# Kernel optimization log

Hardware: AMD Instinct MI355X
Metric: run time of the kernel (lower is better)

Reference implementation:

```python
import jax, jax.numpy as jnp
import numpy as np

B, S, D = 8, 1024, 128
EPS = 1e-7
LN_EPS = 1e-3  # keras LayerNormalization default


def setup_inputs() -> dict:
    key = jax.random.key(0)
    ks = jax.random.split(key, 8)
    sd = 1.0 / np.sqrt(D)
    return {
        "x": jax.random.normal(ks[0], (B, S, D), jnp.float32),
        "Wq": jax.random.normal(ks[1], (D, D), jnp.float32) * sd,
        "bq": jnp.zeros((D,), jnp.float32),
        "Wm": jax.random.normal(ks[2], (D, D), jnp.float32) * sd,
        "bm": jnp.zeros((D,), jnp.float32),
        "Ww": jax.random.normal(ks[3], (D, 1), jnp.float32) * sd,
        "bw": jnp.zeros((1,), jnp.float32),
        "Wc": jax.random.normal(ks[4], (D, 1), jnp.float32) * sd,
        "bc": jnp.zeros((1,), jnp.float32),
        "emb_map": jax.random.normal(ks[5], (D, D, D), jnp.float32) * 0.02,
        "gamma": jnp.ones((D,), jnp.float32),
        "beta": jnp.zeros((D,), jnp.float32),
    }


def reference(x, Wq, bq, Wm, bm, Ww, bw, Wc, bc, emb_map, gamma, beta):
    b_, s_, d_ = x.shape
    q = x @ Wq + bq                      # [B,S,D]
    m = jax.nn.sigmoid(x @ Wm + bm)      # [B,S,D]
    w = jax.nn.relu(x @ Ww + bw)         # [B,S,1]
    c = jax.nn.relu(x @ Wc + bc)         # [B,S,1]

    # distances: for query pos i, preceding pos j (j<i) has distance i-j
    idx = jnp.arange(s_)
    dist = (idx[:, None] - idx[None, :]).astype(x.dtype)   # [S,S]
    valid = dist > 0                                       # strict causal
    # cosh positional decay, zero outside causal window -> [B,S,S]
    pe = jnp.where(valid[None], 1.0 / jnp.cosh((dist[None] - c) / (w + EPS)), 0.0)

    # angle between (pe * x_j * m_i + eps) and (q_i + eps), expanded analytically
    qp = q + EPS
    t1 = jnp.einsum('bjd,bid->bij', x, m * qp)             # sum_d x_j m_i q'_i
    s1 = jnp.einsum('bjd,bid->bij', x, m)                  # sum_d x_j m_i
    s2 = jnp.einsum('bjd,bid->bij', x * x, m * m)          # sum_d (x_j m_i)^2
    dot = pe * t1 + EPS * jnp.sum(qp, axis=-1)[:, :, None]
    na = jnp.sqrt(pe * pe * s2 + 2.0 * EPS * pe * s1 + d_ * EPS * EPS)
    nb = jnp.linalg.norm(qp, axis=-1)[:, :, None]
    cos = jnp.where(valid[None], dot / (na * nb), 0.0)
    angle = jnp.where(valid[None], jnp.arccos(cos), 0.0)   # [B,S,S]

    # query_result_i = sum_j pe*angle * x_j  -> [B,S,D]
    qr = jnp.einsum('bij,bjd->bid', pe * angle, x)

    # embedding matrix: current_token (rows) outer query_result (cols),
    # contracted against rank-3 map: out[b,s,d] = sum_{j,k} x[b,s,j] qr[b,s,k] map[d,j,k]
    em = jnp.einsum('bsj,bsk->bsjk', x, qr).reshape(b_, s_, d_ * d_)
    mapped = em @ emb_map.reshape(d_, d_ * d_).T           # [B,S,D]

    res = mapped + x
    mu = jnp.mean(res, axis=-1, keepdims=True)
    var = jnp.var(res, axis=-1, keepdims=True)
    out = (res - mu) / jnp.sqrt(var + LN_EPS) * gamma + beta
    return out  # dropout is identity at inference
```

## Files before the change

### kernel.cpp

```cpp
#include <hip/hip_runtime.h>
#include <hip/hip_bf16.h>
#include <math.h>

#define DD 128
#define SS 1024
#define NROWS 8192
#define EPSF 1e-7f
#define LN_EPSF 1e-3f
#define TCUT 30.0f

typedef __attribute__((ext_vector_type(8))) short bf16x8;
typedef __attribute__((ext_vector_type(4))) float f32x4;
typedef __attribute__((ext_vector_type(16))) float f32x16;

__device__ __forceinline__ void gload_lds16(const void* g, void* l) {
    __builtin_amdgcn_global_load_lds(
        (const __attribute__((address_space(1))) unsigned int*)g,
        (__attribute__((address_space(3))) unsigned int*)l, 16, 0, 0);
}
__device__ __forceinline__ short f2bf(float v) {
    union { __hip_bfloat16 h; short s; } u;
    u.h = __float2bfloat16(v);
    return u.s;
}
__device__ __forceinline__ float bf2f(short s) {
    union { __hip_bfloat16 h; short s; } u; u.s = s;
    return __bfloat162float(u.h);
}
__device__ __forceinline__ unsigned int pack_bf16(float lo, float hi) {
    unsigned int r;
    asm("v_cvt_pk_bf16_f32 %0, %1, %2" : "=v"(r) : "v"(lo), "v"(hi));
    return r;
}
__device__ __forceinline__ float u2f(unsigned int u) {
    union { unsigned int u; float f; } c; c.u = u; return c.f;
}

__global__ __launch_bounds__(256) void k0a_emb(const float* __restrict__ emb,
                                               short* __restrict__ embh3) {
    __shared__ float lt[32][128];
    int d = blockIdx.x, js = blockIdx.y, t = threadIdx.x;
    {
        int jl = t >> 3, k0 = (t & 7) * 16;
        const float4* src = (const float4*)(emb + (size_t)d * 16384
                                            + (size_t)(js * 32 + jl) * 128 + k0);
#pragma unroll
        for (int q = 0; q < 4; ++q) *(float4*)&lt[jl][k0 + q * 4] = src[q];
    }
    __syncthreads();
    int ks = t >> 5, l0 = (t & 31) * 2;
    union { bf16x8 v[2]; short s[16]; } ob;
#pragma unroll
    for (int li = 0; li < 2; ++li) {
        int l = l0 + li;
        const float* p = &lt[l & 31][ks * 16 + (l >> 5) * 8];
#pragma unroll
        for (int e = 0; e < 8; ++e) ob.s[li * 8 + e] = f2bf(p[e]);
    }
    short* dst = embh3 + (size_t)(d * 4 + js) * 4096 + (size_t)t * 16;
    *(bf16x8*)dst = ob.v[0];
    *(bf16x8*)(dst + 8) = ob.v[1];
}

__global__ __launch_bounds__(256) void k0w_split(const float* __restrict__ Wq,
        const float* __restrict__ Wm, short* __restrict__ Wfrag) {
    int T = blockIdx.x * 256 + threadIdx.x;
    int e = T & 7, l = (T >> 3) & 63, ks = (T >> 9) & 3, nt = (T >> 11) & 7,
        mat = (T >> 14) & 1;
    int k = ks * 32 + ((l >> 4) & 3) * 8 + e;
    int c = nt * 16 + (l & 15);
    float v = (mat ? Wm : Wq)[k * 128 + c];
    short h = f2bf(v);
    float lo = v - bf2f(h);
    Wfrag[((((size_t)(mat * 2 + 0) * 8 + nt) * 4 + ks) * 64 + l) * 8 + e] = h;
    Wfrag[((((size_t)(mat * 2 + 1) * 8 + nt) * 4 + ks) * 64 + l) * 8 + e] = f2bf(lo);
}

__global__ __launch_bounds__(256) void k0c_xsplit(const float* __restrict__ x,
        const float* __restrict__ Ww, const float* __restrict__ bw,
        const float* __restrict__ Wc, const float* __restrict__ bc,
        short* __restrict__ xh2, short* __restrict__ xl2,
        float* __restrict__ scal) {
    __shared__ float xs[32][129];
    int rb = blockIdx.x, t = threadIdx.x;
    {
        int r = t >> 3, d0 = (t & 7) * 16;
        const float4* src = (const float4*)(x + (size_t)(rb * 32 + r) * 128 + d0);
#pragma unroll
        for (int q = 0; q < 4; ++q) *(float4*)&xs[r][d0 + q * 4] = src[q];
    }
    __syncthreads();
    int ks = (t >> 5) & 3, rf = t >> 7, l0 = (t & 31) * 2;
    union { bf16x8 v[2]; short s[16]; } hb, lb;
#pragma unroll
    for (int li = 0; li < 2; ++li) {
        int l = l0 + li;
        const float* p = &xs[rf * 16 + (l & 15)][ks * 32 + ((l >> 4) & 3) * 8];
#pragma unroll
        for (int e = 0; e < 8; ++e) {
            float v = p[e];
            short h = f2bf(v);
            hb.s[li * 8 + e] = h;
            lb.s[li * 8 + e] = f2bf(v - bf2f(h));
        }
    }
    {
        short* d1 = xh2 + (size_t)rb * 4096 + (size_t)t * 16;
        short* d2 = xl2 + (size_t)rb * 4096 + (size_t)t * 16;
        *(bf16x8*)d1 = hb.v[0]; *(bf16x8*)(d1 + 8) = hb.v[1];
        *(bf16x8*)d2 = lb.v[0]; *(bf16x8*)(d2 + 8) = lb.v[1];
    }
    int rr = t >> 3, seg = t & 7;
    float pw = 0.f, pc = 0.f;
#pragma unroll
    for (int dq = 0; dq < 16; ++dq) {
        float xv = xs[rr][seg * 16 + dq];
        pw = fmaf(xv, Ww[seg * 16 + dq], pw);
        pc = fmaf(xv, Wc[seg * 16 + dq], pc);
    }
    pw += __shfl_xor(pw, 1); pw += __shfl_xor(pw, 2); pw += __shfl_xor(pw, 4);
    pc += __shfl_xor(pc, 1); pc += __shfl_xor(pc, 2); pc += __shfl_xor(pc, 4);
    if (seg == 0) {
        scal[(size_t)(rb * 32 + rr) * 4 + 0] = fmaxf(pw + bw[0], 0.f);
        scal[(size_t)(rb * 32 + rr) * 4 + 1] = fmaxf(pc + bc[0], 0.f);
    }
}

__global__ __launch_bounds__(256) void k1_mfma(
    const short* __restrict__ xh2, const short* __restrict__ xl2,
    const short* __restrict__ Wfrag,
    const float* __restrict__ bq, const float* __restrict__ bm,
    float* __restrict__ mq, float* __restrict__ mo, float* __restrict__ scal)
{
    __shared__ __align__(16) short wl[65536];
    __shared__ float red[32][4][2];
    int t = threadIdx.x, w = t >> 6, l = t & 63;
    int l15 = l & 15, g = l >> 4;
    int row0 = blockIdx.x * 32;
#pragma unroll
    for (int it = 0; it < 32; ++it)
        gload_lds16(Wfrag + (size_t)(it * 256 + t) * 8, wl + (size_t)(it * 256 + w * 64) * 8);
    const short* xb  = xh2 + (size_t)blockIdx.x * 4096;
    const short* xlb = xl2 + (size_t)blockIdx.x * 4096;
    bf16x8 Ah[2][4], Al[2][4];
#pragma unroll
    for (int rf = 0; rf < 2; ++rf)
#pragma unroll
        for (int ks = 0; ks < 4; ++ks) {
            size_t o = ((size_t)(rf * 4 + ks) * 64 + l) * 8;
            Ah[rf][ks] = *(const bf16x8*)(xb + o);
            Al[rf][ks] = *(const bf16x8*)(xlb + o);
        }
    __syncthreads();
    f32x4 accq[2][2] = {}, accm[2][2] = {};
#pragma unroll
    for (int ntp = 0; ntp < 2; ++ntp) {
        int nt = w * 2 + ntp;
#pragma unroll
        for (int ks = 0; ks < 4; ++ks) {
            bf16x8 bhq = *(const bf16x8*)(wl + ((size_t)(0  + nt) * 4 + ks) * 512 + l * 8);
            bf16x8 blq = *(const bf16x8*)(wl + ((size_t)(8  + nt) * 4 + ks) * 512 + l * 8);
            bf16x8 bhm = *(const bf16x8*)(wl + ((size_t)(16 + nt) * 4 + ks) * 512 + l * 8);
            bf16x8 blm = *(const bf16x8*)(wl + ((size_t)(24 + nt) * 4 + ks) * 512 + l * 8);
#pragma unroll
            for (int rf = 0; rf < 2; ++rf) {
                accq[rf][ntp] = __builtin_amdgcn_mfma_f32_16x16x32_bf16(Ah[rf][ks], bhq, accq[rf][ntp], 0, 0, 0);
                accq[rf][ntp] = __builtin_amdgcn_mfma_f32_16x16x32_bf16(Ah[rf][ks], blq, accq[rf][ntp], 0, 0, 0);
                accq[rf][ntp] = __builtin_amdgcn_mfma_f32_16x16x32_bf16(Al[rf][ks], bhq, accq[rf][ntp], 0, 0, 0);
                accm[rf][ntp] = __builtin_amdgcn_mfma_f32_16x16x32_bf16(Ah[rf][ks], bhm, accm[rf][ntp], 0, 0, 0);
                accm[rf][ntp] = __builtin_amdgcn_mfma_f32_16x16x32_bf16(Ah[rf][ks], blm, accm[rf][ntp], 0, 0, 0);
                accm[rf][ntp] = __builtin_amdgcn_mfma_f32_16x16x32_bf16(Al[rf][ks], bhm, accm[rf][ntp], 0, 0, 0);
            }
        }
    }
    float sq1[2][4] = {{0,0,0,0},{0,0,0,0}};
    float sq2[2][4] = {{0,0,0,0},{0,0,0,0}};
#pragma unroll
    for (int ntp = 0; ntp < 2; ++ntp) {
        int c = (w * 2 + ntp) * 16 + l15;
        float bqv = bq[c] + EPSF, bmv = bm[c];
#pragma unroll
        for (int rf = 0; rf < 2; ++rf)
#pragma unroll
            for (int reg = 0; reg < 4; ++reg) {
                int rloc = rf * 16 + g * 4 + reg;
                float qp = accq[rf][ntp][reg] + bqv;
                float mv = 1.0f / (1.0f + expf(-(accm[rf][ntp][reg] + bmv)));
                size_t o = (size_t)(row0 + rloc) * 128 + c;
                mq[o] = mv * qp;
                mo[o] = mv;
                sq1[rf][reg] += qp;
                sq2[rf][reg] += qp * qp;
            }
    }
#pragma unroll
    for (int rf = 0; rf < 2; ++rf)
#pragma unroll
        for (int reg = 0; reg < 4; ++reg) {
            float a = sq1[rf][reg], b = sq2[rf][reg];
            a += __shfl_xor(a, 1); a += __shfl_xor(a, 2);
            a += __shfl_xor(a, 4); a += __shfl_xor(a, 8);
            b += __shfl_xor(b, 1); b += __shfl_xor(b, 2);
            b += __shfl_xor(b, 4); b += __shfl_xor(b, 8);
            if (l15 == 0) {
                red[rf * 16 + g * 4 + reg][w][0] = a;
                red[rf * 16 + g * 4 + reg][w][1] = b;
            }
        }
    __syncthreads();
    if (t < 32) {
        float a = red[t][0][0] + red[t][1][0] + red[t][2][0] + red[t][3][0];
        float b = red[t][0][1] + red[t][1][1] + red[t][2][1] + red[t][3][1];
        scal[(size_t)(row0 + t) * 4 + 2] = a;
        scal[(size_t)(row0 + t) * 4 + 3] = sqrtf(b);
    }
}

__global__ __launch_bounds__(256) void k2_qr(
    const float* __restrict__ x,
    const float* __restrict__ mq, const float* __restrict__ mo,
    const float* __restrict__ scal, short* __restrict__ qrh2)
{
    int row = blockIdx.x;
    int i = row & (SS - 1);
    const float* xb = x + (size_t)(row - i) * DD;
    int t = threadIdx.x, w = t >> 6, l = t & 63;
    int sub = l >> 4, q = l & 15;
    int qo = q * 8;

    float mqv[8], mov[8];
    {
        const float* mp = mq + (size_t)row * DD + qo;
        float4 a = *(const float4*)mp, b = *(const float4*)(mp + 4);
        mqv[0] = a.x; mqv[1] = a.y; mqv[2] = a.z; mqv[3] = a.w;
        mqv[4] = b.x; mqv[5] = b.y; mqv[6] = b.z; mqv[7] = b.w;
        const float* op = mo + (size_t)row * DD + qo;
        float4 c = *(const float4*)op, d = *(const float4*)(op + 4);
        mov[0] = c.x; mov[1] = c.y; mov[2] = c.z; mov[3] = c.w;
        mov[4] = d.x; mov[5] = d.y; mov[6] = d.z; mov[7] = d.w;
    }
    float wv = scal[row * 4 + 0], cv = scal[row * 4 + 1];
    float sumqp = scal[row * 4 + 2], nb = scal[row * 4 + 3];
    float wi = wv + EPSF;
    float dmaxf = cv + TCUT * wi;
    int dmax = (dmaxf >= (float)i) ? i : (int)dmaxf;

    float acc[8] = {0.f, 0.f, 0.f, 0.f, 0.f, 0.f, 0.f, 0.f};
    int nit = (dmax + 15) >> 4;
    int dbase = 1 + w * 4 + sub;
    for (int it = 0; it < nit; ++it) {
        int dist = dbase + it * 16;
        float xv[8];
        if (dist <= dmax) {
            const float* xp = xb + (size_t)(i - dist) * DD + qo;
            float4 a = *(const float4*)xp, b = *(const float4*)(xp + 4);
            xv[0] = a.x; xv[1] = a.y; xv[2] = a.z; xv[3] = a.w;
            xv[4] = b.x; xv[5] = b.y; xv[6] = b.z; xv[7] = b.w;
        } else {
#pragma unroll
            for (int e = 0; e < 8; ++e) xv[e] = 0.f;
        }
        float t1 = 0.f, s1 = 0.f, s2 = 0.f;
#pragma unroll
        for (int e = 0; e < 8; ++e) {
            float xm = xv[e] * mov[e];
            t1 = fmaf(xv[e], mqv[e], t1);
            s1 += xm;
            s2 = fmaf(xm, xm, s2);
        }
#pragma unroll
        for (int off = 1; off < 16; off <<= 1) {
            t1 += __shfl_xor(t1, off);
            s1 += __shfl_xor(s1, off);
            s2 += __shfl_xor(s2, off);
        }
        float tt = ((float)dist - cv) / wi;
        float pe = 1.0f / coshf(tt);
        float dotv = fmaf(pe, t1, EPSF * sumqp);
        float na = sqrtf(fmaf(pe * pe, s2,
                         fmaf(2.0f * EPSF * pe, s1, (float)DD * EPSF * EPSF)));
        float cosv = fminf(1.0f, fmaxf(-1.0f, dotv / (na * nb)));
        float ang = acosf(cosv);
        float wgt = pe * ang;
#pragma unroll
        for (int e = 0; e < 8; ++e) acc[e] = fmaf(wgt, xv[e], acc[e]);
    }
#pragma unroll
    for (int e = 0; e < 8; ++e) {
        acc[e] += __shfl_xor(acc[e], 16);
        acc[e] += __shfl_xor(acc[e], 32);
    }
    __shared__ float sq[4][DD];
    if (l < 16) {
#pragma unroll
        for (int e = 0; e < 8; ++e) sq[w][qo + e] = acc[e];
    }
    __syncthreads();
    if (t < DD) {
        float v = sq[0][t] + sq[1][t] + sq[2][t] + sq[3][t];
        int rbq = row >> 7, rr = row & 127, rt2 = rr >> 5, lp = rr & 31;
        int k = t;
        qrh2[(((size_t)(rbq * 4 + rt2) * 8 + (k >> 4)) * 64
              + (lp + 32 * ((k >> 3) & 1))) * 8 + (k & 7)] = f2bf(v);
    }
}

__global__ __launch_bounds__(256, 2) void k3_gemm(
    const float* __restrict__ x, const short* __restrict__ embh3,
    const short* __restrict__ qrh2, float* __restrict__ part)
{
    __shared__ __align__(16) char ldsb[65536];
    short* xtwh = (short*)ldsb;
    short* elds = (short*)ldsb;
    float* sof  = (float*)ldsb;

    int t = threadIdx.x, w = t >> 6, l = t & 63;
    int l31 = l & 31, hi = l >> 5;
    int rc = blockIdx.x, dq = blockIdx.y, js = blockIdx.z;

#pragma unroll
    for (int i = 0; i < 8; ++i) {
        int idx = i * 256 + t;
        int r = idx >> 3, j4 = (idx & 7) * 4;
        float4 v = *(const float4*)(x + (size_t)(rc * 256 + r) * 128 + js * 32 + j4);
        *(unsigned int*)(xtwh + r * 36 + j4)     = pack_bf16(v.x, v.y);
        *(unsigned int*)(xtwh + r * 36 + j4 + 2) = pack_bf16(v.z, v.w);
    }

    bf16x8 Bf[2][8];
#pragma unroll
    for (int rt = 0; rt < 2; ++rt) {
        int R32 = rc * 8 + w * 2 + rt;
#pragma unroll
        for (int s = 0; s < 8; ++s)
            Bf[rt][s] = *(const bf16x8*)(qrh2
                + (((size_t)R32 * 8 + s) * 64 + l) * 8);
    }

    __syncthreads();

    float xv[2][16];
#pragma unroll
    for (int rt = 0; rt < 2; ++rt) {
        int row_l = w * 64 + rt * 32 + l31;
#pragma unroll
        for (int p = 0; p < 8; ++p) {
            int jA = ((2 * p) & 3) + 8 * (p >> 1) + 4 * hi;
            unsigned int u = *(const unsigned int*)(xtwh + row_l * 36 + jA);
            xv[rt][2 * p]     = u2f(u << 16);
            xv[rt][2 * p + 1] = u2f(u & 0xFFFF0000u);
        }
    }

    __syncthreads();

#pragma unroll
    for (int i = 0; i < 16; ++i) {
        int c = i * 256 + t;
        int d = c >> 9, off = c & 511;
        gload_lds16(embh3 + (size_t)((dq * 8 + d) * 4 + js) * 4096 + (size_t)off * 8,
                    elds + (size_t)(i * 256 + w * 64) * 8);
    }
    __syncthreads();

    float sout[2][8];

#pragma unroll
    for (int d = 0; d < 8; ++d) {
        bf16x8 A[8];
#pragma unroll
        for (int s = 0; s < 8; ++s)
            A[s] = *(const bf16x8*)(elds + d * 4096 + (s * 64 + l) * 8);
#pragma unroll
        for (int rt = 0; rt < 2; ++rt) {
            f32x16 acc;
#pragma unroll
            for (int q = 0; q < 16; ++q) acc[q] = 0.f;
#pragma unroll
            for (int s = 0; s < 8; ++s)
                acc = __builtin_amdgcn_mfma_f32_32x32x16_bf16(A[s], Bf[rt][s],
                                                              acc, 0, 0, 0);
            float s0 = 0.f, s1 = 0.f, s2 = 0.f, s3 = 0.f;
#pragma unroll
            for (int q = 0; q < 4; ++q) {
                s0 = fmaf(xv[rt][q * 4 + 0], acc[q * 4 + 0], s0);
                s1 = fmaf(xv[rt][q * 4 + 1], acc[q * 4 + 1], s1);
                s2 = fmaf(xv[rt][q * 4 + 2], acc[q * 4 + 2], s2);
                s3 = fmaf(xv[rt][q * 4 + 3], acc[q * 4 + 3], s3);
            }
            float sm = (s0 + s1) + (s2 + s3);
            sm += __shfl_xor(sm, 32);
            sout[rt][d] = sm;
        }
    }

    __syncthreads();
    if (hi == 0) {
#pragma unroll
        for (int rt = 0; rt < 2; ++rt)
#pragma unroll
            for (int d = 0; d < 8; ++d)
                sof[(w * 64 + rt * 32 + l31) * 8 + d] = sout[rt][d];
    }
    __syncthreads();

#pragma unroll
    for (int i = 0; i < 2; ++i) {
        int idx = i * 256 + t;
        int r = idx >> 1, q = (idx & 1) * 4;
        float4 v = *(const float4*)&sof[r * 8 + q];
        *(float4*)(part + (size_t)js * (NROWS * DD)
                   + (size_t)(rc * 256 + r) * 128 + dq * 8 + q) = v;
    }
}

__global__ __launch_bounds__(256) void k4_ln(
    const float* __restrict__ x, const float* __restrict__ part,
    const float* __restrict__ gamma, const float* __restrict__ beta,
    float* __restrict__ out)
{
    int wave = threadIdx.x >> 6, lane = threadIdx.x & 63;
    int row = blockIdx.x * 4 + wave;
    size_t base = (size_t)row * DD;
    float r0 = x[base + lane], r1 = x[base + lane + 64];
#pragma unroll
    for (int p = 0; p < 4; ++p) {
        r0 += part[(size_t)p * NROWS * DD + base + lane];
        r1 += part[(size_t)p * NROWS * DD + base + lane + 64];
    }
    float s = r0 + r1, s2 = r0 * r0 + r1 * r1;
#pragma unroll
    for (int off = 32; off > 0; off >>= 1) {
        s += __shfl_xor(s, off);
        s2 += __shfl_xor(s2, off);
    }
    float mu = s * (1.0f / DD);
    float var = s2 * (1.0f / DD) - mu * mu;
    var = fmaxf(var, 0.0f);
    float rs = rsqrtf(var + LN_EPSF);
    out[base + lane] = (r0 - mu) * rs * gamma[lane] + beta[lane];
    out[base + lane + 64] = (r1 - mu) * rs * gamma[lane + 64] + beta[lane + 64];
}

extern "C" void kernel_launch(void* const* d_in, const int* in_sizes, int n_in,
                              void* d_out, int out_size, void* d_ws, size_t ws_size,
                              hipStream_t stream) {
    const float* x     = (const float*)d_in[0];
    const float* Wq    = (const float*)d_in[1];
    const float* bq    = (const float*)d_in[2];
    const float* Wm    = (const float*)d_in[3];
    const float* bm    = (const float*)d_in[4];
    const float* Ww    = (const float*)d_in[5];
    const float* bw    = (const float*)d_in[6];
    const float* Wc    = (const float*)d_in[7];
    const float* bc    = (const float*)d_in[8];
    const float* emb   = (const float*)d_in[9];
    const float* gamma = (const float*)d_in[10];
    const float* beta  = (const float*)d_in[11];
    float* out = (float*)d_out;
    float* ws  = (float*)d_ws;

    short* embh3 = (short*)ws;
    short* qrh2  = (short*)(ws + 1048576);
    float* scal  = ws + 1572864;
    float* part  = ws + 1605632;
    float* tr    = ws + 1605632;
    short* xh2   = (short*)tr;
    short* xl2   = (short*)(tr + 524288);
    float* mq    = tr + 1048576;
    float* mo    = tr + 2097152;
    short* Wfrag = (short*)(tr + 3145728);

    hipLaunchKernelGGL(k0a_emb,   dim3(128, 4), dim3(256), 0, stream, emb, embh3);
    hipLaunchKernelGGL(k0w_split, dim3(256),    dim3(256), 0, stream, Wq, Wm, Wfrag);
    hipLaunchKernelGGL(k0c_xsplit,dim3(256),    dim3(256), 0, stream,
                       x, Ww, bw, Wc, bc, xh2, xl2, scal);
    hipLaunchKernelGGL(k1_mfma,   dim3(256),    dim3(256), 0, stream,
                       xh2, xl2, Wfrag, bq, bm, mq, mo, scal);
    hipLaunchKernelGGL(k2_qr,     dim3(8192),   dim3(256), 0, stream,
                       x, mq, mo, scal, qrh2);
    hipLaunchKernelGGL(k3_gemm,   dim3(32, 16, 4), dim3(256), 0, stream,
                       x, embh3, qrh2, part);
    hipLaunchKernelGGL(k4_ln,     dim3(2048),   dim3(256), 0, stream,
                       x, part, gamma, beta, out);
}
```

Before: 90.87 us.

## Halve k3 output tile per block to raise occupancy and drop LDS staging of x

Each k3_gemm block now handles 4 output columns instead of 8, cutting LDS to 32KB plus a small staging buffer, and doubles the grid in the dq dimension. Launch bounds ask for 4 blocks per CU instead of 2. x is read straight from global memory into registers as fp32, replacing the bf16 LDS round-trip, and the emb load starts first with no extra barriers. The trade-off is that the qr B-fragments and x values are reloaded twice as often across blocks, and there is more register pressure under the tighter launch bound.

New measurement: 220.5 us. 143% more time.

```diff
diff --git a/kernel.cpp b/kernel.cpp
--- a/kernel.cpp
+++ b/kernel.cpp
@@ -26,14 +26,6 @@
 __device__ __forceinline__ float bf2f(short s) {
     union { __hip_bfloat16 h; short s; } u; u.s = s;
     return __bfloat162float(u.h);
-}
-__device__ __forceinline__ unsigned int pack_bf16(float lo, float hi) {
-    unsigned int r;
-    asm("v_cvt_pk_bf16_f32 %0, %1, %2" : "=v"(r) : "v"(lo), "v"(hi));
-    return r;
-}
-__device__ __forceinline__ float u2f(unsigned int u) {
-    union { unsigned int u; float f; } c; c.u = u; return c.f;
 }
 
 __global__ __launch_bounds__(256) void k0a_emb(const float* __restrict__ emb,
@@ -305,26 +297,22 @@
     }
 }
 
-__global__ __launch_bounds__(256, 2) void k3_gemm(
+__global__ __launch_bounds__(256, 4) void k3_gemm(
     const float* __restrict__ x, const short* __restrict__ embh3,
     const short* __restrict__ qrh2, float* __restrict__ part)
 {
-    __shared__ __align__(16) char ldsb[65536];
-    short* xtwh = (short*)ldsb;
-    short* elds = (short*)ldsb;
-    float* sof  = (float*)ldsb;
-
+    __shared__ __align__(16) short elds[4 * 4096];
+    __shared__ float sof[256 * 4];
     int t = threadIdx.x, w = t >> 6, l = t & 63;
     int l31 = l & 31, hi = l >> 5;
     int rc = blockIdx.x, dq = blockIdx.y, js = blockIdx.z;
 
 #pragma unroll
     for (int i = 0; i < 8; ++i) {
-        int idx = i * 256 + t;
-        int r = idx >> 3, j4 = (idx & 7) * 4;
-        float4 v = *(const float4*)(x + (size_t)(rc * 256 + r) * 128 + js * 32 + j4);
-        *(unsigned int*)(xtwh + r * 36 + j4)     = pack_bf16(v.x, v.y);
-        *(unsigned int*)(xtwh + r * 36 + j4 + 2) = pack_bf16(v.z, v.w);
+        int c = i * 256 + t;
+        int d = c >> 9, off = c & 511;
+        gload_lds16(embh3 + (size_t)((dq * 4 + d) * 4 + js) * 4096 + (size_t)off * 8,
+                    elds + (size_t)(i * 256 + w * 64) * 8);
     }
 
     bf16x8 Bf[2][8];
@@ -333,40 +321,28 @@
         int R32 = rc * 8 + w * 2 + rt;
 #pragma unroll
         for (int s = 0; s < 8; ++s)
-            Bf[rt][s] = *(const bf16x8*)(qrh2
-                + (((size_t)R32 * 8 + s) * 64 + l) * 8);
-    }
-
-    __syncthreads();
+            Bf[rt][s] = *(const bf16x8*)(qrh2 + (((size_t)R32 * 8 + s) * 64 + l) * 8);
+    }
 
     float xv[2][16];
 #pragma unroll
     for (int rt = 0; rt < 2; ++rt) {
-        int row_l = w * 64 + rt * 32 + l31;
-#pragma unroll
-        for (int p = 0; p < 8; ++p) {
-            int jA = ((2 * p) & 3) + 8 * (p >> 1) + 4 * hi;
-            unsigned int u = *(const unsigned int*)(xtwh + row_l * 36 + jA);
-            xv[rt][2 * p]     = u2f(u << 16);
-            xv[rt][2 * p + 1] = u2f(u & 0xFFFF0000u);
-        }
-    }
-
-    __syncthreads();
-
-#pragma unroll
-    for (int i = 0; i < 16; ++i) {
-        int c = i * 256 + t;
-        int d = c >> 9, off = c & 511;
-        gload_lds16(embh3 + (size_t)((dq * 8 + d) * 4 + js) * 4096 + (size_t)off * 8,
-                    elds + (size_t)(i * 256 + w * 64) * 8);
-    }
-    __syncthreads();
-
-    float sout[2][8];
-
-#pragma unroll
-    for (int d = 0; d < 8; ++d) {
+        int row = rc * 256 + w * 64 + rt * 32 + l31;
+#pragma unroll
+        for (int g4 = 0; g4 < 4; ++g4) {
+            float4 v = *(const float4*)(x + (size_t)row * 128 + js * 32 + g4 * 8 + 4 * hi);
+            xv[rt][g4 * 4 + 0] = v.x;
+            xv[rt][g4 * 4 + 1] = v.y;
+            xv[rt][g4 * 4 + 2] = v.z;
+            xv[rt][g4 * 4 + 3] = v.w;
+        }
+    }
+
+    __syncthreads();
+
+    float sout[2][4];
+#pragma unroll
+    for (int d = 0; d < 4; ++d) {
         bf16x8 A[8];
 #pragma unroll
         for (int s = 0; s < 8; ++s)
@@ -399,18 +375,15 @@
 #pragma unroll
         for (int rt = 0; rt < 2; ++rt)
 #pragma unroll
-            for (int d = 0; d < 8; ++d)
-                sof[(w * 64 + rt * 32 + l31) * 8 + d] = sout[rt][d];
-    }
-    __syncthreads();
-
-#pragma unroll
-    for (int i = 0; i < 2; ++i) {
-        int idx = i * 256 + t;
-        int r = idx >> 1, q = (idx & 1) * 4;
-        float4 v = *(const float4*)&sof[r * 8 + q];
+            for (int d = 0; d < 4; ++d)
+                sof[(w * 64 + rt * 32 + l31) * 4 + d] = sout[rt][d];
+    }
+    __syncthreads();
+
+    {
+        float4 v = *(const float4*)&sof[t * 4];
         *(float4*)(part + (size_t)js * (NROWS * DD)
-                   + (size_t)(rc * 256 + r) * 128 + dq * 8 + q) = v;
+                   + (size_t)(rc * 256 + t) * 128 + dq * 4) = v;
     }
 }
 
@@ -479,7 +452,7 @@
                        xh2, xl2, Wfrag, bq, bm, mq, mo, scal);
     hipLaunchKernelGGL(k2_qr,     dim3(8192),   dim3(256), 0, stream,
                        x, mq, mo, scal, qrh2);
-    hipLaunchKernelGGL(k3_gemm,   dim3(32, 16, 4), dim3(256), 0, stream,
+    hipLaunchKernelGGL(k3_gemm,   dim3(32, 32, 4), dim3(256), 0, stream,
                        x, embh3, qrh2, part);
     hipLaunchKernelGGL(k4_ln,     dim3(2048),   dim3(256), 0, stream,
                        x, part, gamma, beta, out);
```

## Double-buffer emb_map tiles in k3 GEMM, split K across waves, store bf16 partials

Applied to the files above, without the earlier changes.

The k3 embedding GEMM now loops over 8 stages of 4 output columns per block, double-buffering emb_map tiles in LDS so the next tile loads while the current one is computed. Each wave takes half of the K dimension and 4 row tiles, which reuses each A fragment across more MFMAs. The grid shrinks from 16 to 4 column groups. Partial sums are written as packed bf16 pairs into 8 partial buffers, which k4_ln sums. This cuts the global traffic of the partial stores but adds bf16 rounding to the partial sums and doubles the number of partials read in layernorm.

Result: slower. 98.45 us (+8.3%).

```diff
diff --git a/kernel.cpp b/kernel.cpp
--- a/kernel.cpp
+++ b/kernel.cpp
@@ -307,115 +307,124 @@
 
 __global__ __launch_bounds__(256, 2) void k3_gemm(
     const float* __restrict__ x, const short* __restrict__ embh3,
-    const short* __restrict__ qrh2, float* __restrict__ part)
+    const short* __restrict__ qrh2, short* __restrict__ partb)
 {
-    __shared__ __align__(16) char ldsb[65536];
-    short* xtwh = (short*)ldsb;
-    short* elds = (short*)ldsb;
-    float* sof  = (float*)ldsb;
+    __shared__ __align__(16) short elds[2][16384];
+    short* xtwh = &elds[0][0];
 
     int t = threadIdx.x, w = t >> 6, l = t & 63;
     int l31 = l & 31, hi = l >> 5;
-    int rc = blockIdx.x, dq = blockIdx.y, js = blockIdx.z;
+    int kp = w & 1, rh = w >> 1;
+    int rc = blockIdx.x, dqb = blockIdx.y, js = blockIdx.z;
 
 #pragma unroll
     for (int i = 0; i < 8; ++i) {
         int idx = i * 256 + t;
         int r = idx >> 3, j4 = (idx & 7) * 4;
         float4 v = *(const float4*)(x + (size_t)(rc * 256 + r) * 128 + js * 32 + j4);
-        *(unsigned int*)(xtwh + r * 36 + j4)     = pack_bf16(v.x, v.y);
-        *(unsigned int*)(xtwh + r * 36 + j4 + 2) = pack_bf16(v.z, v.w);
-    }
-
-    bf16x8 Bf[2][8];
-#pragma unroll
-    for (int rt = 0; rt < 2; ++rt) {
-        int R32 = rc * 8 + w * 2 + rt;
-#pragma unroll
-        for (int s = 0; s < 8; ++s)
+        *(unsigned int*)(xtwh + r * 34 + j4)     = pack_bf16(v.x, v.y);
+        *(unsigned int*)(xtwh + r * 34 + j4 + 2) = pack_bf16(v.z, v.w);
+    }
+
+    {
+        int dgb = dqb * 32;
+#pragma unroll
+        for (int i = 0; i < 8; ++i) {
+            int c = i * 256 + t;
+            int d = c >> 9, off = c & 511;
+            gload_lds16(embh3 + (size_t)((dgb + d) * 4 + js) * 4096 + (size_t)off * 8,
+                        &elds[1][0] + (size_t)(i * 256 + w * 64) * 8);
+        }
+    }
+
+    bf16x8 Bf[4][4];
+#pragma unroll
+    for (int rt = 0; rt < 4; ++rt) {
+        int R32 = rc * 8 + rh * 4 + rt;
+#pragma unroll
+        for (int s = 0; s < 4; ++s)
             Bf[rt][s] = *(const bf16x8*)(qrh2
-                + (((size_t)R32 * 8 + s) * 64 + l) * 8);
-    }
-
-    __syncthreads();
-
-    float xv[2][16];
-#pragma unroll
-    for (int rt = 0; rt < 2; ++rt) {
-        int row_l = w * 64 + rt * 32 + l31;
+                + (((size_t)R32 * 8 + kp * 4 + s) * 64 + l) * 8);
+    }
+
+    __syncthreads();
+
+    unsigned int xvp[4][8];
+#pragma unroll
+    for (int rt = 0; rt < 4; ++rt) {
+        int row_l = rh * 128 + rt * 32 + l31;
 #pragma unroll
         for (int p = 0; p < 8; ++p) {
             int jA = ((2 * p) & 3) + 8 * (p >> 1) + 4 * hi;
-            unsigned int u = *(const unsigned int*)(xtwh + row_l * 36 + jA);
-            xv[rt][2 * p]     = u2f(u << 16);
-            xv[rt][2 * p + 1] = u2f(u & 0xFFFF0000u);
-        }
-    }
-
-    __syncthreads();
-
-#pragma unroll
-    for (int i = 0; i < 16; ++i) {
-        int c = i * 256 + t;
-        int d = c >> 9, off = c & 511;
-        gload_lds16(embh3 + (size_t)((dq * 8 + d) * 4 + js) * 4096 + (size_t)off * 8,
-                    elds + (size_t)(i * 256 + w * 64) * 8);
-    }
-    __syncthreads();
-
-    float sout[2][8];
-
-#pragma unroll
-    for (int d = 0; d < 8; ++d) {
-        bf16x8 A[8];
-#pragma unroll
-        for (int s = 0; s < 8; ++s)
-            A[s] = *(const bf16x8*)(elds + d * 4096 + (s * 64 + l) * 8);
-#pragma unroll
-        for (int rt = 0; rt < 2; ++rt) {
-            f32x16 acc;
-#pragma unroll
-            for (int q = 0; q < 16; ++q) acc[q] = 0.f;
-#pragma unroll
-            for (int s = 0; s < 8; ++s)
-                acc = __builtin_amdgcn_mfma_f32_32x32x16_bf16(A[s], Bf[rt][s],
-                                                              acc, 0, 0, 0);
-            float s0 = 0.f, s1 = 0.f, s2 = 0.f, s3 = 0.f;
-#pragma unroll
-            for (int q = 0; q < 4; ++q) {
-                s0 = fmaf(xv[rt][q * 4 + 0], acc[q * 4 + 0], s0);
-                s1 = fmaf(xv[rt][q * 4 + 1], acc[q * 4 + 1], s1);
-                s2 = fmaf(xv[rt][q * 4 + 2], acc[q * 4 + 2], s2);
-                s3 = fmaf(xv[rt][q * 4 + 3], acc[q * 4 + 3], s3);
+            xvp[rt][p] = *(const unsigned int*)(xtwh + row_l * 34 + jA);
+        }
+    }
+    __syncthreads();
+
+    size_t pbase = (size_t)(js * 2 + kp) * ((size_t)NROWS * DD);
+    float sprev[4];
+
+#pragma unroll 1
+    for (int st = 0; st < 8; ++st) {
+        if (st < 7) {
+            int dgb = dqb * 32 + (st + 1) * 4;
+            short* dstb = &elds[st & 1][0];
+#pragma unroll
+            for (int i = 0; i < 8; ++i) {
+                int c = i * 256 + t;
+                int d = c >> 9, off = c & 511;
+                gload_lds16(embh3 + (size_t)((dgb + d) * 4 + js) * 4096 + (size_t)off * 8,
+                            dstb + (size_t)(i * 256 + w * 64) * 8);
             }
-            float sm = (s0 + s1) + (s2 + s3);
-            sm += __shfl_xor(sm, 32);
-            sout[rt][d] = sm;
-        }
-    }
-
-    __syncthreads();
-    if (hi == 0) {
-#pragma unroll
-        for (int rt = 0; rt < 2; ++rt)
-#pragma unroll
-            for (int d = 0; d < 8; ++d)
-                sof[(w * 64 + rt * 32 + l31) * 8 + d] = sout[rt][d];
-    }
-    __syncthreads();
-
-#pragma unroll
-    for (int i = 0; i < 2; ++i) {
-        int idx = i * 256 + t;
-        int r = idx >> 1, q = (idx & 1) * 4;
-        float4 v = *(const float4*)&sof[r * 8 + q];
-        *(float4*)(part + (size_t)js * (NROWS * DD)
-                   + (size_t)(rc * 256 + r) * 128 + dq * 8 + q) = v;
+        }
+        const short* eb = &elds[(st + 1) & 1][0];
+
+#pragma unroll
+        for (int dloc = 0; dloc < 4; ++dloc) {
+            bf16x8 A[4];
+#pragma unroll
+            for (int s = 0; s < 4; ++s)
+                A[s] = *(const bf16x8*)(eb + dloc * 4096 + ((kp * 4 + s) * 64 + l) * 8);
+            f32x16 acc[4];
+#pragma unroll
+            for (int rt = 0; rt < 4; ++rt)
+#pragma unroll
+                for (int q = 0; q < 16; ++q) acc[rt][q] = 0.f;
+#pragma unroll
+            for (int s = 0; s < 4; ++s)
+#pragma unroll
+                for (int rt = 0; rt < 4; ++rt)
+                    acc[rt] = __builtin_amdgcn_mfma_f32_32x32x16_bf16(
+                        A[s], Bf[rt][s], acc[rt], 0, 0, 0);
+#pragma unroll
+            for (int rt = 0; rt < 4; ++rt) {
+                float s0 = 0.f, s1 = 0.f, s2 = 0.f, s3 = 0.f;
+#pragma unroll
+                for (int p = 0; p < 8; p += 2) {
+                    unsigned int u0 = xvp[rt][p], u1 = xvp[rt][p + 1];
+                    s0 = fmaf(u2f(u0 << 16),          acc[rt][2 * p],     s0);
+                    s1 = fmaf(u2f(u0 & 0xFFFF0000u),  acc[rt][2 * p + 1], s1);
+                    s2 = fmaf(u2f(u1 << 16),          acc[rt][2 * p + 2], s2);
+                    s3 = fmaf(u2f(u1 & 0xFFFF0000u),  acc[rt][2 * p + 3], s3);
+                }
+                float sm = (s0 + s1) + (s2 + s3);
+                sm += __shfl_xor(sm, 32);
+                if ((dloc & 1) == 0) {
+                    sprev[rt] = sm;
+                } else if (hi == 0) {
+                    int row_g = rc * 256 + rh * 128 + rt * 32 + l31;
+                    int dg = dqb * 32 + st * 4 + (dloc - 1);
+                    *(unsigned int*)(partb + pbase + (size_t)row_g * 128 + dg)
+                        = pack_bf16(sprev[rt], sm);
+                }
+            }
+        }
+        __syncthreads();
     }
 }
 
 __global__ __launch_bounds__(256) void k4_ln(
-    const float* __restrict__ x, const float* __restrict__ part,
+    const float* __restrict__ x, const short* __restrict__ partb,
     const float* __restrict__ gamma, const float* __restrict__ beta,
     float* __restrict__ out)
 {
@@ -424,9 +433,9 @@
     size_t base = (size_t)row * DD;
     float r0 = x[base + lane], r1 = x[base + lane + 64];
 #pragma unroll
-    for (int p = 0; p < 4; ++p) {
-        r0 += part[(size_t)p * NROWS * DD + base + lane];
-        r1 += part[(size_t)p * NROWS * DD + base + lane + 64];
+    for (int p = 0; p < 8; ++p) {
+        r0 += bf2f(partb[(size_t)p * 1048576 + base + lane]);
+        r1 += bf2f(partb[(size_t)p * 1048576 + base + lane + 64]);
     }
     float s = r0 + r1, s2 = r0 * r0 + r1 * r1;
 #pragma unroll
@@ -463,7 +472,7 @@
     short* embh3 = (short*)ws;
     short* qrh2  = (short*)(ws + 1048576);
     float* scal  = ws + 1572864;
-    float* part  = ws + 1605632;
+    short* partb = (short*)(ws + 1605632);
     float* tr    = ws + 1605632;
     short* xh2   = (short*)tr;
     short* xl2   = (short*)(tr + 524288);
@@ -479,8 +488,8 @@
                        xh2, xl2, Wfrag, bq, bm, mq, mo, scal);
     hipLaunchKernelGGL(k2_qr,     dim3(8192),   dim3(256), 0, stream,
                        x, mq, mo, scal, qrh2);
-    hipLaunchKernelGGL(k3_gemm,   dim3(32, 16, 4), dim3(256), 0, stream,
-                       x, embh3, qrh2, part);
+    hipLaunchKernelGGL(k3_gemm,   dim3(32, 4, 4), dim3(256), 0, stream,
+                       x, embh3, qrh2, partb);
     hipLaunchKernelGGL(k4_ln,     dim3(2048),   dim3(256), 0, stream,
-                       x, part, gamma, beta, out);
-}
+                       x, partb, gamma, beta, out);
+}
```

## Restructure embedding GEMM to scale qr by x and contract over full d

Applied to the files above, without the earlier changes.

The bilinear embedding contraction is reformulated. Previously each block computed per-d MFMAs of emb against qr and then reduced with x in registers, across a 32x16x4 grid. Now the A operand is formed by scaling qr by x_j on the fly, and each block accumulates over 32 j values with emb B-fragments streamed from global memory through double-buffered registers. Each block produces full 64-row by 128-column outputs, and the two k-halves are reduced through LDS. This is meant to cut redundant MFMA epilogue work and LDS staging, at the cost of extra per-iteration VALU packing and bf16 rounding of the product x*qr.

After: 89.52 us. About the same (-1.5%).

```diff
diff --git a/kernel.cpp b/kernel.cpp
--- a/kernel.cpp
+++ b/kernel.cpp
@@ -37,29 +37,27 @@
 }
 
 __global__ __launch_bounds__(256) void k0a_emb(const float* __restrict__ emb,
-                                               short* __restrict__ embh3) {
-    __shared__ float lt[32][128];
-    int d = blockIdx.x, js = blockIdx.y, t = threadIdx.x;
+                                               short* __restrict__ embB) {
+    __shared__ float lt[128][132];
+    int j = blockIdx.x, t = threadIdx.x;
     {
-        int jl = t >> 3, k0 = (t & 7) * 16;
-        const float4* src = (const float4*)(emb + (size_t)d * 16384
-                                            + (size_t)(js * 32 + jl) * 128 + k0);
-#pragma unroll
-        for (int q = 0; q < 4; ++q) *(float4*)&lt[jl][k0 + q * 4] = src[q];
-    }
-    __syncthreads();
-    int ks = t >> 5, l0 = (t & 31) * 2;
-    union { bf16x8 v[2]; short s[16]; } ob;
-#pragma unroll
-    for (int li = 0; li < 2; ++li) {
-        int l = l0 + li;
-        const float* p = &lt[l & 31][ks * 16 + (l >> 5) * 8];
-#pragma unroll
-        for (int e = 0; e < 8; ++e) ob.s[li * 8 + e] = f2bf(p[e]);
-    }
-    short* dst = embh3 + (size_t)(d * 4 + js) * 4096 + (size_t)t * 16;
-    *(bf16x8*)dst = ob.v[0];
-    *(bf16x8*)(dst + 8) = ob.v[1];
+        int d = t >> 1, kh = (t & 1) * 64;
+        const float* src = emb + (size_t)d * 16384 + (size_t)j * 128 + kh;
+#pragma unroll
+        for (int q = 0; q < 16; ++q)
+            *(float4*)&lt[d][kh + q * 4] = *(const float4*)(src + q * 4);
+    }
+    __syncthreads();
+#pragma unroll
+    for (int i = 0; i < 8; ++i) {
+        int idx = i * 256 + t;
+        int l = idx & 63, s = (idx >> 6) & 7, dt = (idx >> 9) & 3;
+        const float* p = &lt[dt * 32 + (l & 31)][s * 16 + (l >> 5) * 8];
+        union { bf16x8 v; short sa[8]; } ob;
+#pragma unroll
+        for (int e = 0; e < 8; ++e) ob.sa[e] = f2bf(p[e]);
+        *(bf16x8*)(embB + (size_t)j * 16384 + dt * 4096 + s * 512 + (size_t)l * 8) = ob.v;
+    }
 }
 
 __global__ __launch_bounds__(256) void k0w_split(const float* __restrict__ Wq,
@@ -306,111 +304,133 @@
 }
 
 __global__ __launch_bounds__(256, 2) void k3_gemm(
-    const float* __restrict__ x, const short* __restrict__ embh3,
+    const float* __restrict__ x, const short* __restrict__ embB,
     const short* __restrict__ qrh2, float* __restrict__ part)
 {
-    __shared__ __align__(16) char ldsb[65536];
-    short* xtwh = (short*)ldsb;
-    short* elds = (short*)ldsb;
-    float* sof  = (float*)ldsb;
-
+    __shared__ float xt[32][68];
+    __shared__ float sof[64][128];
     int t = threadIdx.x, w = t >> 6, l = t & 63;
     int l31 = l & 31, hi = l >> 5;
-    int rc = blockIdx.x, dq = blockIdx.y, js = blockIdx.z;
-
+    int dh = w & 1, sh = w >> 1;
+    int rb = blockIdx.x, js = blockIdx.y;
+
+    {
+        int r = t >> 2, q = t & 3;
+        const float* xp = x + (size_t)(rb * 64 + r) * 128 + js * 32 + q * 8;
+        float4 a = *(const float4*)xp, b = *(const float4*)(xp + 4);
+        xt[q * 8 + 0][r] = a.x; xt[q * 8 + 1][r] = a.y;
+        xt[q * 8 + 2][r] = a.z; xt[q * 8 + 3][r] = a.w;
+        xt[q * 8 + 4][r] = b.x; xt[q * 8 + 5][r] = b.y;
+        xt[q * 8 + 6][r] = b.z; xt[q * 8 + 7][r] = b.w;
+    }
+
+    unsigned int qrp[2][4][4];
+#pragma unroll
+    for (int rt = 0; rt < 2; ++rt) {
+        int R32 = rb * 2 + rt;
+#pragma unroll
+        for (int s = 0; s < 4; ++s) {
+            union { bf16x8 v; unsigned int u[4]; } qb;
+            qb.v = *(const bf16x8*)(qrh2
+                + (((size_t)R32 * 8 + sh * 4 + s) * 64 + l) * 8);
+#pragma unroll
+            for (int p = 0; p < 4; ++p) qrp[rt][s][p] = qb.u[p];
+        }
+    }
+
+    const short* Bbase = embB + (size_t)(js * 32) * 16384
+                         + (size_t)(dh * 2) * 4096 + (size_t)(sh * 4) * 512
+                         + (size_t)l * 8;
+
+    f32x16 acc[2][2];
+#pragma unroll
+    for (int rt = 0; rt < 2; ++rt)
+#pragma unroll
+        for (int i = 0; i < 2; ++i)
+#pragma unroll
+            for (int q = 0; q < 16; ++q) acc[rt][i][q] = 0.f;
+
+#define LOADB(BN, JJ)                                                       \
+    {                                                                       \
+        const short* bp_ = Bbase + (size_t)(JJ) * 16384;                    \
+        _Pragma("unroll")                                                   \
+        for (int i = 0; i < 2; ++i)                                         \
+            _Pragma("unroll")                                               \
+            for (int s = 0; s < 4; ++s)                                     \
+                BN[i][s] = *(const bf16x8*)(bp_ + i * 4096 + s * 512);      \
+    }
+
+#define COMPUTE(BN, JJ)                                                     \
+    {                                                                       \
+        float xs0 = xt[JJ][l31], xs1 = xt[JJ][32 + l31];                    \
+        _Pragma("unroll")                                                   \
+        for (int s = 0; s < 4; ++s) {                                       \
+            union { bf16x8 v; unsigned int u[4]; } a0, a1;                  \
+            _Pragma("unroll")                                               \
+            for (int p = 0; p < 4; ++p) {                                   \
+                unsigned int q0 = qrp[0][s][p], q1 = qrp[1][s][p];          \
+                a0.u[p] = pack_bf16(u2f(q0 << 16) * xs0,                    \
+                                    u2f(q0 & 0xFFFF0000u) * xs0);           \
+                a1.u[p] = pack_bf16(u2f(q1 << 16) * xs1,                    \
+                                    u2f(q1 & 0xFFFF0000u) * xs1);           \
+            }                                                               \
+            acc[0][0] = __builtin_amdgcn_mfma_f32_32x32x16_bf16(            \
+                a0.v, BN[0][s], acc[0][0], 0, 0, 0);                        \
+            acc[0][1] = __builtin_amdgcn_mfma_f32_32x32x16_bf16(            \
+                a0.v, BN[1][s], acc[0][1], 0, 0, 0);                        \
+            acc[1][0] = __builtin_amdgcn_mfma_f32_32x32x16_bf16(            \
+                a1.v, BN[0][s], acc[1][0], 0, 0, 0);                        \
+            acc[1][1] = __builtin_amdgcn_mfma_f32_32x32x16_bf16(            \
+                a1.v, BN[1][s], acc[1][1], 0, 0, 0);                        \
+        }                                                                   \
+    }
+
+    bf16x8 B0[2][4], B1[2][4];
+    LOADB(B0, 0)
+    __syncthreads();
+
+#pragma unroll 1
+    for (int jj = 0; jj < 32; jj += 2) {
+        if (jj + 1 < 32) LOADB(B1, jj + 1)
+        COMPUTE(B0, jj)
+        if (jj + 2 < 32) LOADB(B0, jj + 2)
+        COMPUTE(B1, jj + 1)
+    }
+#undef LOADB
+#undef COMPUTE
+
+    __syncthreads();
+    if (sh == 0) {
+#pragma unroll
+        for (int rt = 0; rt < 2; ++rt)
+#pragma unroll
+            for (int i = 0; i < 2; ++i)
+#pragma unroll
+                for (int q = 0; q < 16; ++q) {
+                    int r = rt * 32 + (q & 3) + 8 * (q >> 2) + 4 * hi;
+                    sof[r][(dh * 2 + i) * 32 + l31] = acc[rt][i][q];
+                }
+    }
+    __syncthreads();
+    if (sh == 1) {
+#pragma unroll
+        for (int rt = 0; rt < 2; ++rt)
+#pragma unroll
+            for (int i = 0; i < 2; ++i)
+#pragma unroll
+                for (int q = 0; q < 16; ++q) {
+                    int r = rt * 32 + (q & 3) + 8 * (q >> 2) + 4 * hi;
+                    sof[r][(dh * 2 + i) * 32 + l31] += acc[rt][i][q];
+                }
+    }
+    __syncthreads();
 #pragma unroll
     for (int i = 0; i < 8; ++i) {
         int idx = i * 256 + t;
-        int r = idx >> 3, j4 = (idx & 7) * 4;
-        float4 v = *(const float4*)(x + (size_t)(rc * 256 + r) * 128 + js * 32 + j4);
-        *(unsigned int*)(xtwh + r * 36 + j4)     = pack_bf16(v.x, v.y);
-        *(unsigned int*)(xtwh + r * 36 + j4 + 2) = pack_bf16(v.z, v.w);
-    }
-
-    bf16x8 Bf[2][8];
-#pragma unroll
-    for (int rt = 0; rt < 2; ++rt) {
-        int R32 = rc * 8 + w * 2 + rt;
-#pragma unroll
-        for (int s = 0; s < 8; ++s)
-            Bf[rt][s] = *(const bf16x8*)(qrh2
-                + (((size_t)R32 * 8 + s) * 64 + l) * 8);
-    }
-
-    __syncthreads();
-
-    float xv[2][16];
-#pragma unroll
-    for (int rt = 0; rt < 2; ++rt) {
-        int row_l = w * 64 + rt * 32 + l31;
-#pragma unroll
-        for (int p = 0; p < 8; ++p) {
-            int jA = ((2 * p) & 3) + 8 * (p >> 1) + 4 * hi;
-            unsigned int u = *(const unsigned int*)(xtwh + row_l * 36 + jA);
-            xv[rt][2 * p]     = u2f(u << 16);
-            xv[rt][2 * p + 1] = u2f(u & 0xFFFF0000u);
-        }
-    }
-
-    __syncthreads();
-
-#pragma unroll
-    for (int i = 0; i < 16; ++i) {
-        int c = i * 256 + t;
-        int d = c >> 9, off = c & 511;
-        gload_lds16(embh3 + (size_t)((dq * 8 + d) * 4 + js) * 4096 + (size_t)off * 8,
-                    elds + (size_t)(i * 256 + w * 64) * 8);
-    }
-    __syncthreads();
-
-    float sout[2][8];
-
-#pragma unroll
-    for (int d = 0; d < 8; ++d) {
-        bf16x8 A[8];
-#pragma unroll
-        for (int s = 0; s < 8; ++s)
-            A[s] = *(const bf16x8*)(elds + d * 4096 + (s * 64 + l) * 8);
-#pragma unroll
-        for (int rt = 0; rt < 2; ++rt) {
-            f32x16 acc;
-#pragma unroll
-            for (int q = 0; q < 16; ++q) acc[q] = 0.f;
-#pragma unroll
-            for (int s = 0; s < 8; ++s)
-                acc = __builtin_amdgcn_mfma_f32_32x32x16_bf16(A[s], Bf[rt][s],
-                                                              acc, 0, 0, 0);
-            float s0 = 0.f, s1 = 0.f, s2 = 0.f, s3 = 0.f;
-#pragma unroll
-            for (int q = 0; q < 4; ++q) {
-                s0 = fmaf(xv[rt][q * 4 + 0], acc[q * 4 + 0], s0);
-                s1 = fmaf(xv[rt][q * 4 + 1], acc[q * 4 + 1], s1);
-                s2 = fmaf(xv[rt][q * 4 + 2], acc[q * 4 + 2], s2);
-                s3 = fmaf(xv[rt][q * 4 + 3], acc[q * 4 + 3], s3);
-            }
-            float sm = (s0 + s1) + (s2 + s3);
-            sm += __shfl_xor(sm, 32);
-            sout[rt][d] = sm;
-        }
-    }
-
-    __syncthreads();
-    if (hi == 0) {
-#pragma unroll
-        for (int rt = 0; rt < 2; ++rt)
-#pragma unroll
-            for (int d = 0; d < 8; ++d)
-                sof[(w * 64 + rt * 32 + l31) * 8 + d] = sout[rt][d];
-    }
-    __syncthreads();
-
-#pragma unroll
-    for (int i = 0; i < 2; ++i) {
-        int idx = i * 256 + t;
-        int r = idx >> 1, q = (idx & 1) * 4;
-        float4 v = *(const float4*)&sof[r * 8 + q];
+        int r = idx >> 5, c4 = (idx & 31) * 4;
+        float4 v = *(const float4*)&sof[r][c4];
         *(float4*)(part + (size_t)js * (NROWS * DD)
-                   + (size_t)(rc * 256 + r) * 128 + dq * 8 + q) = v;
+                   + (size_t)(rb * 64 + r) * 128 + c4) = v;
     }
 }
 
@@ -460,7 +480,7 @@
     float* out = (float*)d_out;
     float* ws  = (float*)d_ws;
 
-    short* embh3 = (short*)ws;
+    short* embB  = (short*)ws;
     short* qrh2  = (short*)(ws + 1048576);
     float* scal  = ws + 1572864;
     float* part  = ws + 1605632;
@@ -471,7 +491,7 @@
     float* mo    = tr + 2097152;
     short* Wfrag = (short*)(tr + 3145728);
 
-    hipLaunchKernelGGL(k0a_emb,   dim3(128, 4), dim3(256), 0, stream, emb, embh3);
+    hipLaunchKernelGGL(k0a_emb,   dim3(128),    dim3(256), 0, stream, emb, embB);
     hipLaunchKernelGGL(k0w_split, dim3(256),    dim3(256), 0, stream, Wq, Wm, Wfrag);
     hipLaunchKernelGGL(k0c_xsplit,dim3(256),    dim3(256), 0, stream,
                        x, Ww, bw, Wc, bc, xh2, xl2, scal);
@@ -479,8 +499,8 @@
                        xh2, xl2, Wfrag, bq, bm, mq, mo, scal);
     hipLaunchKernelGGL(k2_qr,     dim3(8192),   dim3(256), 0, stream,
                        x, mq, mo, scal, qrh2);
-    hipLaunchKernelGGL(k3_gemm,   dim3(32, 16, 4), dim3(256), 0, stream,
-                       x, embh3, qrh2, part);
+    hipLaunchKernelGGL(k3_gemm,   dim3(128, 4), dim3(256), 0, stream,
+                       x, embB, qrh2, part);
     hipLaunchKernelGGL(k4_ln,     dim3(2048),   dim3(256), 0, stream,
                        x, part, gamma, beta, out);
 }
```
